# Optimization experiments

Measured on AMD Instinct MI355X. Metric: run time of the kernel, lower is better.

## Reference

```python
import jax, jax.numpy as jnp
import numpy as np

NUM_HEADS = 16
WINDOW = 256
DIM = 1024


def setup_inputs() -> dict:
    key = jax.random.key(0)
    k1, k2, k3, k4, k5 = jax.random.split(key, 5)
    B, L, D = 2, 2048, DIM
    s = 1.0 / np.sqrt(D)
    return {
        "x": jax.random.normal(k1, (B, L, D), dtype=jnp.float32),
        "in_proj_w": jax.random.uniform(k2, (3 * D, D), dtype=jnp.float32, minval=-s, maxval=s),
        "in_proj_b": jax.random.uniform(k3, (3 * D,), dtype=jnp.float32, minval=-s, maxval=s),
        "out_w": jax.random.uniform(k4, (D, D), dtype=jnp.float32, minval=-s, maxval=s),
        "out_b": jax.random.uniform(k5, (D,), dtype=jnp.float32, minval=-s, maxval=s),
    }


def reference(x, in_proj_w, in_proj_b, out_w, out_b):
    B, L, D = x.shape
    H = NUM_HEADS
    hd = D // H

    # combined qkv projection, as in nn.MultiheadAttention
    qkv = x @ in_proj_w.T + in_proj_b          # [B, L, 3D]
    q, k, v = jnp.split(qkv, 3, axis=-1)
    q = q.reshape(B, L, H, hd).transpose(0, 2, 1, 3)  # [B, H, L, hd]
    k = k.reshape(B, L, H, hd).transpose(0, 2, 1, 3)
    v = v.reshape(B, L, H, hd).transpose(0, 2, 1, 3)

    scale = 1.0 / jnp.sqrt(jnp.asarray(hd, dtype=x.dtype))
    scores = jnp.einsum("bhqd,bhkd->bhqk", q * scale, k)  # [B, H, L, L]

    # sliding-window causal mask: allowed iff i-window < j <= i
    i = jnp.arange(L)[:, None]
    j = jnp.arange(L)[None, :]
    allowed = (j <= i) & (j > i - WINDOW)                  # [L, L]
    scores = jnp.where(allowed[None, None], scores, -jnp.inf)

    attn = jax.nn.softmax(scores, axis=-1)
    out = jnp.einsum("bhqk,bhkd->bhqd", attn, v)           # [B, H, L, hd]
    out = out.transpose(0, 2, 1, 3).reshape(B, L, D)
    return out @ out_w.T + out_b
```

## Files before the change

### kernel.cpp

```cpp
#include <hip/hip_runtime.h>


#define SEQ_L 2048
#define WIN   256

typedef __bf16 bf16x8 __attribute__((ext_vector_type(8)));
typedef float  f32x4  __attribute__((ext_vector_type(4)));

__device__ __forceinline__ unsigned short f32_to_bf16(float f) {
  unsigned int u = __float_as_uint(f);
  u += 0x7FFFu + ((u >> 16) & 1u);
  return (unsigned short)(u >> 16);
}

__device__ __forceinline__ void async16(const unsigned short* g, unsigned short* l) {
  __builtin_amdgcn_global_load_lds(
      (const __attribute__((address_space(1))) unsigned int*)g,
      (__attribute__((address_space(3))) unsigned int*)l, 16, 0, 0);
}

__global__ void cast_all(const float* __restrict__ x,  unsigned short* __restrict__ xo,
                         const float* __restrict__ w1, unsigned short* __restrict__ w1o,
                         const float* __restrict__ w2, unsigned short* __restrict__ w2o) {
  int i = blockIdx.x * 256 + threadIdx.x;
  const float* in; unsigned short* out; int k;
  if (i < 1048576)       { in = x;  out = xo;  k = i; }
  else if (i < 1835008)  { in = w1; out = w1o; k = i - 1048576; }
  else                   { in = w2; out = w2o; k = i - 1835008; }
  float4 v = ((const float4*)in)[k];
  ushort4 o;
  o.x = f32_to_bf16(v.x); o.y = f32_to_bf16(v.y);
  o.z = f32_to_bf16(v.z); o.w = f32_to_bf16(v.w);
  ((ushort4*)out)[k] = o;
}

template<int TBM, int TBN, int MI, int NI, int OUTBF>
__global__ __launch_bounds__(256) void gemm_nt(
    const unsigned short* __restrict__ A,
    const unsigned short* __restrict__ Bt,
    const float* __restrict__ bias,
    void* __restrict__ Cout, int M, int N, int K)
{
  __shared__ unsigned short As[TBM * 64];
  __shared__ unsigned short Bs[TBN * 64];

  const int tid  = threadIdx.x;
  const int lane = tid & 63;
  const int wave = tid >> 6;
  const int wr   = (wave >> 1) * (MI * 16);
  const int wc   = (wave & 1) * (NI * 16);
  const int quad = lane >> 4;
  const int l16  = lane & 15;
  const int lrow = lane >> 3;
  const int scol = (lane & 7) ^ lrow;

  const long m0 = (long)blockIdx.y * TBM;
  const long n0 = (long)blockIdx.x * TBN;

  f32x4 acc[MI][NI];
#pragma unroll
  for (int i = 0; i < MI; ++i)
#pragma unroll
    for (int j = 0; j < NI; ++j)
#pragma unroll
      for (int r = 0; r < 4; ++r) acc[i][j][r] = 0.0f;

  for (int k0 = 0; k0 < K; k0 += 64) {
#pragma unroll
    for (int p = 0; p < TBM / 32; ++p) {
      int rb = wave * (TBM / 4) + p * 8;
      async16(A + (m0 + rb + lrow) * (long)K + k0 + scol * 8, &As[rb * 64]);
    }
#pragma unroll
    for (int p = 0; p < TBN / 32; ++p) {
      int rb = wave * (TBN / 4) + p * 8;
      async16(Bt + (n0 + rb + lrow) * (long)K + k0 + scol * 8, &Bs[rb * 64]);
    }
    __syncthreads();
#pragma unroll
    for (int ks = 0; ks < 2; ++ks) {
      bf16x8 af[MI], bfv[NI];
#pragma unroll
      for (int mi = 0; mi < MI; ++mi) {
        int r = wr + mi * 16 + l16;
        af[mi] = *(const bf16x8*)(&As[r * 64 + ((ks * 4 + quad) ^ (r & 7)) * 8]);
      }
#pragma unroll
      for (int ni = 0; ni < NI; ++ni) {
        int r = wc + ni * 16 + l16;
        bfv[ni] = *(const bf16x8*)(&Bs[r * 64 + ((ks * 4 + quad) ^ (r & 7)) * 8]);
      }
#pragma unroll
      for (int mi = 0; mi < MI; ++mi)
#pragma unroll
        for (int ni = 0; ni < NI; ++ni)
          acc[mi][ni] = __builtin_amdgcn_mfma_f32_16x16x32_bf16(af[mi], bfv[ni], acc[mi][ni], 0, 0, 0);
    }
    __syncthreads();
  }

#pragma unroll
  for (int ni = 0; ni < NI; ++ni) {
    long col = n0 + wc + ni * 16 + l16;
    float bv = bias[col];
#pragma unroll
    for (int mi = 0; mi < MI; ++mi) {
      long rowb = m0 + wr + mi * 16 + quad * 4;
#pragma unroll
      for (int r = 0; r < 4; ++r) {
        float v = acc[mi][ni][r] + bv;
        if (OUTBF) ((unsigned short*)Cout)[(rowb + r) * N + col] = f32_to_bf16(v);
        else       ((float*)Cout)[(rowb + r) * N + col] = v;
      }
    }
  }
}

__global__ __launch_bounds__(256) void attn_kernel(
    const unsigned short* __restrict__ qkv,
    unsigned short* __restrict__ aout)
{
  __shared__ unsigned short Ks[64 * 72];
  __shared__ unsigned short Vt[64 * 72];
  __shared__ unsigned short Ps[4 * 16 * 72];

  const int tid  = threadIdx.x;
  const int w    = tid >> 6;
  const int lane = tid & 63;
  const int quad = lane >> 4;
  const int l16  = lane & 15;

  const int blk = blockIdx.x;
  const int qt  = blk & 31;
  const int h   = (blk >> 5) & 15;
  const int b   = blk >> 9;

  const int  i0  = qt * 64;
  const int  i0w = i0 + w * 16;
  const long rowbase = (long)b * SEQ_L;
  const float NEG_INF = -__builtin_inff();

  bf16x8 aq[2];
  {
    const unsigned short* qp = qkv + (rowbase + i0w + l16) * 3072 + h * 64 + quad * 8;
    aq[0] = *(const bf16x8*)(qp);
    aq[1] = *(const bf16x8*)(qp + 32);
  }

  f32x4 o[4];
#pragma unroll
  for (int ni = 0; ni < 4; ++ni)
#pragma unroll
    for (int r = 0; r < 4; ++r) o[ni][r] = 0.0f;
  float m_i[4], l_i[4];
#pragma unroll
  for (int r = 0; r < 4; ++r) { m_i[r] = NEG_INF; l_i[r] = 0.0f; }

  unsigned short* psw = &Ps[w * 16 * 72];

  const int j_begin = (i0 >= WIN) ? i0 - WIN : 0;

  for (int j0 = j_begin; j0 <= i0; j0 += 64) {
    __syncthreads();
#pragma unroll
    for (int p = 0; p < 2; ++p) {
      int c = p * 256 + tid, row = c >> 3, col8 = c & 7;
      const unsigned short* base = qkv + (rowbase + j0 + row) * 3072 + h * 64 + col8 * 8;
      *(uint4*)(&Ks[row * 72 + col8 * 8]) = *(const uint4*)(base + 1024);
      unsigned short tmp[8];
      *(uint4*)tmp = *(const uint4*)(base + 2048);
      int rsw = row ^ (col8 << 3);
#pragma unroll
      for (int e = 0; e < 8; ++e)
        Vt[(col8 * 8 + e) * 72 + rsw] = tmp[e];
    }
    __syncthreads();

    f32x4 s[4];
#pragma unroll
    for (int g = 0; g < 4; ++g) {
      bf16x8 k0 = *(const bf16x8*)(&Ks[(g * 16 + l16) * 72 + quad * 8]);
      bf16x8 k1 = *(const bf16x8*)(&Ks[(g * 16 + l16) * 72 + 32 + quad * 8]);
      f32x4 z;
#pragma unroll
      for (int r = 0; r < 4; ++r) z[r] = 0.0f;
      z = __builtin_amdgcn_mfma_f32_16x16x32_bf16(aq[0], k0, z, 0, 0, 0);
      z = __builtin_amdgcn_mfma_f32_16x16x32_bf16(aq[1], k1, z, 0, 0, 0);
      s[g] = z;
    }
#pragma unroll
    for (int g = 0; g < 4; ++g) {
      int j = j0 + g * 16 + l16;
#pragma unroll
      for (int r = 0; r < 4; ++r) {
        int i = i0w + quad * 4 + r;
        float sv = s[g][r] * 0.125f;
        bool ok = (j <= i) && (j > i - WIN);
        s[g][r] = ok ? sv : NEG_INF;
      }
    }
    float alpha[4];
#pragma unroll
    for (int r = 0; r < 4; ++r) {
      float mx = fmaxf(fmaxf(s[0][r], s[1][r]), fmaxf(s[2][r], s[3][r]));
      mx = fmaxf(mx, __shfl_xor(mx, 1));
      mx = fmaxf(mx, __shfl_xor(mx, 2));
      mx = fmaxf(mx, __shfl_xor(mx, 4));
      mx = fmaxf(mx, __shfl_xor(mx, 8));
      float m_new = fmaxf(m_i[r], mx);
      float a = (m_new == NEG_INF) ? 1.0f : __expf(m_i[r] - m_new);
      float rs = 0.0f;
#pragma unroll
      for (int g = 0; g < 4; ++g) {
        float e = (s[g][r] == NEG_INF) ? 0.0f : __expf(s[g][r] - m_new);
        psw[(quad * 4 + r) * 72 + g * 16 + l16] = f32_to_bf16(e);
        rs += e;
      }
      rs += __shfl_xor(rs, 1);
      rs += __shfl_xor(rs, 2);
      rs += __shfl_xor(rs, 4);
      rs += __shfl_xor(rs, 8);
      l_i[r] = l_i[r] * a + rs;
      m_i[r] = m_new;
      alpha[r] = a;
#pragma unroll
      for (int ni = 0; ni < 4; ++ni) o[ni][r] *= a;
    }
    asm volatile("s_waitcnt lgkmcnt(0)" ::: "memory");
#pragma unroll
    for (int kk = 0; kk < 2; ++kk) {
      bf16x8 ap = *(const bf16x8*)(&psw[l16 * 72 + kk * 32 + quad * 8]);
#pragma unroll
      for (int ni = 0; ni < 4; ++ni) {
        int d  = ni * 16 + l16;
        int rb = (kk * 32 + quad * 8) ^ (((d >> 3) & 7) << 3);
        bf16x8 bv = *(const bf16x8*)(&Vt[d * 72 + rb]);
        o[ni] = __builtin_amdgcn_mfma_f32_16x16x32_bf16(ap, bv, o[ni], 0, 0, 0);
      }
    }
  }

#pragma unroll
  for (int r = 0; r < 4; ++r) {
    float inv_l = 1.0f / l_i[r];
    long row = rowbase + i0w + quad * 4 + r;
#pragma unroll
    for (int ni = 0; ni < 4; ++ni)
      aout[row * 1024 + h * 64 + ni * 16 + l16] = f32_to_bf16(o[ni][r] * inv_l);
  }
}

extern "C" void kernel_launch(void* const* d_in, const int* in_sizes, int n_in,
                              void* d_out, int out_size, void* d_ws, size_t ws_size,
                              hipStream_t stream)
{
  const float* x  = (const float*)d_in[0];
  const float* w1 = (const float*)d_in[1];
  const float* b1 = (const float*)d_in[2];
  const float* w2 = (const float*)d_in[3];
  const float* b2 = (const float*)d_in[4];
  float* out = (float*)d_out;

  char* ws = (char*)d_ws;
  unsigned short* x_bf   = (unsigned short*)(ws);
  unsigned short* w1_bf  = (unsigned short*)(ws + 8388608);
  unsigned short* w2_bf  = (unsigned short*)(ws + 14680064);
  unsigned short* qkv_bf = (unsigned short*)(ws + 16777216);
  unsigned short* at_bf  = (unsigned short*)(ws + 41943040);

  cast_all<<<8192, 256, 0, stream>>>(x, x_bf, w1, w1_bf, w2, w2_bf);

  dim3 g1(3072 / 128, 4096 / 128);
  gemm_nt<128, 128, 4, 4, 1><<<g1, 256, 0, stream>>>(x_bf, w1_bf, b1, qkv_bf, 4096, 3072, 1024);

  attn_kernel<<<1024, 256, 0, stream>>>(qkv_bf, at_bf);

  dim3 g2(1024 / 64, 4096 / 128);
  gemm_nt<128, 64, 4, 2, 0><<<g2, 256, 0, stream>>>(at_bf, w2_bf, b2, out, 4096, 1024, 1024);
}
```

Before: 170.0 us.

## Process two query sub-tiles per attention block, drop online max, retile output GEMM

Each attention block now covers 128 query rows in two 64-row sub-tiles, so every K/V tile loaded into LDS is reused by both sub-tiles and the block count is halved. Fully masked sub-tile/key-tile pairs are skipped. The online softmax max tracking and rescaling are removed and exponentials are taken directly on scaled scores, which relies on the scores staying small enough not to overflow. The output projection GEMM moves to 64x64 tiles, giving more blocks.

Result: faster. 164.1 us (-3.4%).

```diff
diff --git a/kernel.cpp b/kernel.cpp
--- a/kernel.cpp
+++ b/kernel.cpp
@@ -131,36 +131,36 @@
   const int l16  = lane & 15;
 
   const int blk = blockIdx.x;
-  const int qt  = blk & 31;
-  const int h   = (blk >> 5) & 15;
-  const int b   = blk >> 9;
-
-  const int  i0  = qt * 64;
-  const int  i0w = i0 + w * 16;
+  const int qb  = blk & 15;
+  const int h   = (blk >> 4) & 15;
+  const int b   = blk >> 8;
+
+  const int  i0 = qb * 128;
   const long rowbase = (long)b * SEQ_L;
-  const float NEG_INF = -__builtin_inff();
-
-  bf16x8 aq[2];
-  {
-    const unsigned short* qp = qkv + (rowbase + i0w + l16) * 3072 + h * 64 + quad * 8;
-    aq[0] = *(const bf16x8*)(qp);
-    aq[1] = *(const bf16x8*)(qp + 32);
-  }
-
-  f32x4 o[4];
-#pragma unroll
-  for (int ni = 0; ni < 4; ++ni)
-#pragma unroll
-    for (int r = 0; r < 4; ++r) o[ni][r] = 0.0f;
-  float m_i[4], l_i[4];
-#pragma unroll
-  for (int r = 0; r < 4; ++r) { m_i[r] = NEG_INF; l_i[r] = 0.0f; }
+
+  bf16x8 aq[2][2];
+#pragma unroll
+  for (int sub = 0; sub < 2; ++sub) {
+    const unsigned short* qp =
+        qkv + (rowbase + i0 + sub * 64 + w * 16 + l16) * 3072 + h * 64 + quad * 8;
+    aq[sub][0] = *(const bf16x8*)(qp);
+    aq[sub][1] = *(const bf16x8*)(qp + 32);
+  }
+
+  f32x4 o[2][4];
+  float l_i[2][4];
+#pragma unroll
+  for (int sub = 0; sub < 2; ++sub)
+#pragma unroll
+    for (int ni = 0; ni < 4; ++ni)
+#pragma unroll
+      for (int r = 0; r < 4; ++r) { o[sub][ni][r] = 0.0f; l_i[sub][r] = 0.0f; }
 
   unsigned short* psw = &Ps[w * 16 * 72];
 
   const int j_begin = (i0 >= WIN) ? i0 - WIN : 0;
 
-  for (int j0 = j_begin; j0 <= i0; j0 += 64) {
+  for (int j0 = j_begin; j0 < i0 + 128; j0 += 64) {
     __syncthreads();
 #pragma unroll
     for (int p = 0; p < 2; ++p) {
@@ -176,78 +176,76 @@
     }
     __syncthreads();
 
-    f32x4 s[4];
+    bf16x8 kf[4][2];
 #pragma unroll
     for (int g = 0; g < 4; ++g) {
-      bf16x8 k0 = *(const bf16x8*)(&Ks[(g * 16 + l16) * 72 + quad * 8]);
-      bf16x8 k1 = *(const bf16x8*)(&Ks[(g * 16 + l16) * 72 + 32 + quad * 8]);
-      f32x4 z;
-#pragma unroll
-      for (int r = 0; r < 4; ++r) z[r] = 0.0f;
-      z = __builtin_amdgcn_mfma_f32_16x16x32_bf16(aq[0], k0, z, 0, 0, 0);
-      z = __builtin_amdgcn_mfma_f32_16x16x32_bf16(aq[1], k1, z, 0, 0, 0);
-      s[g] = z;
-    }
-#pragma unroll
-    for (int g = 0; g < 4; ++g) {
-      int j = j0 + g * 16 + l16;
-#pragma unroll
-      for (int r = 0; r < 4; ++r) {
-        int i = i0w + quad * 4 + r;
-        float sv = s[g][r] * 0.125f;
-        bool ok = (j <= i) && (j > i - WIN);
-        s[g][r] = ok ? sv : NEG_INF;
-      }
-    }
-    float alpha[4];
+      kf[g][0] = *(const bf16x8*)(&Ks[(g * 16 + l16) * 72 + quad * 8]);
+      kf[g][1] = *(const bf16x8*)(&Ks[(g * 16 + l16) * 72 + 32 + quad * 8]);
+    }
+    bf16x8 vf[2][4];
+#pragma unroll
+    for (int kk = 0; kk < 2; ++kk)
+#pragma unroll
+      for (int ni = 0; ni < 4; ++ni) {
+        int d  = ni * 16 + l16;
+        int rb = (kk * 32 + quad * 8) ^ (((d >> 3) & 7) << 3);
+        vf[kk][ni] = *(const bf16x8*)(&Vt[d * 72 + rb]);
+      }
+
+#pragma unroll
+    for (int sub = 0; sub < 2; ++sub) {
+      const int i0s = i0 + sub * 64 + w * 16;
+      if (j0 > i0s + 15) continue;
+      if (j0 + 63 + WIN <= i0s) continue;
+
+      f32x4 s[4];
+#pragma unroll
+      for (int g = 0; g < 4; ++g) {
+        f32x4 z;
+#pragma unroll
+        for (int r = 0; r < 4; ++r) z[r] = 0.0f;
+        z = __builtin_amdgcn_mfma_f32_16x16x32_bf16(aq[sub][0], kf[g][0], z, 0, 0, 0);
+        z = __builtin_amdgcn_mfma_f32_16x16x32_bf16(aq[sub][1], kf[g][1], z, 0, 0, 0);
+        s[g] = z;
+      }
+#pragma unroll
+      for (int g = 0; g < 4; ++g) {
+        int j = j0 + g * 16 + l16;
+#pragma unroll
+        for (int r = 0; r < 4; ++r) {
+          int i = i0s + quad * 4 + r;
+          bool ok = (j <= i) && (j > i - WIN);
+          float e = ok ? __expf(s[g][r] * 0.125f) : 0.0f;
+          psw[(quad * 4 + r) * 72 + g * 16 + l16] = f32_to_bf16(e);
+          l_i[sub][r] += e;
+        }
+      }
+      asm volatile("s_waitcnt lgkmcnt(0)" ::: "memory");
+#pragma unroll
+      for (int kk = 0; kk < 2; ++kk) {
+        bf16x8 ap = *(const bf16x8*)(&psw[l16 * 72 + kk * 32 + quad * 8]);
+#pragma unroll
+        for (int ni = 0; ni < 4; ++ni)
+          o[sub][ni] = __builtin_amdgcn_mfma_f32_16x16x32_bf16(ap, vf[kk][ni], o[sub][ni], 0, 0, 0);
+      }
+    }
+  }
+
+#pragma unroll
+  for (int sub = 0; sub < 2; ++sub)
 #pragma unroll
     for (int r = 0; r < 4; ++r) {
-      float mx = fmaxf(fmaxf(s[0][r], s[1][r]), fmaxf(s[2][r], s[3][r]));
-      mx = fmaxf(mx, __shfl_xor(mx, 1));
-      mx = fmaxf(mx, __shfl_xor(mx, 2));
-      mx = fmaxf(mx, __shfl_xor(mx, 4));
-      mx = fmaxf(mx, __shfl_xor(mx, 8));
-      float m_new = fmaxf(m_i[r], mx);
-      float a = (m_new == NEG_INF) ? 1.0f : __expf(m_i[r] - m_new);
-      float rs = 0.0f;
-#pragma unroll
-      for (int g = 0; g < 4; ++g) {
-        float e = (s[g][r] == NEG_INF) ? 0.0f : __expf(s[g][r] - m_new);
-        psw[(quad * 4 + r) * 72 + g * 16 + l16] = f32_to_bf16(e);
-        rs += e;
-      }
+      float rs = l_i[sub][r];
       rs += __shfl_xor(rs, 1);
       rs += __shfl_xor(rs, 2);
       rs += __shfl_xor(rs, 4);
       rs += __shfl_xor(rs, 8);
-      l_i[r] = l_i[r] * a + rs;
-      m_i[r] = m_new;
-      alpha[r] = a;
-#pragma unroll
-      for (int ni = 0; ni < 4; ++ni) o[ni][r] *= a;
-    }
-    asm volatile("s_waitcnt lgkmcnt(0)" ::: "memory");
-#pragma unroll
-    for (int kk = 0; kk < 2; ++kk) {
-      bf16x8 ap = *(const bf16x8*)(&psw[l16 * 72 + kk * 32 + quad * 8]);
-#pragma unroll
-      for (int ni = 0; ni < 4; ++ni) {
-        int d  = ni * 16 + l16;
-        int rb = (kk * 32 + quad * 8) ^ (((d >> 3) & 7) << 3);
-        bf16x8 bv = *(const bf16x8*)(&Vt[d * 72 + rb]);
-        o[ni] = __builtin_amdgcn_mfma_f32_16x16x32_bf16(ap, bv, o[ni], 0, 0, 0);
-      }
-    }
-  }
-
-#pragma unroll
-  for (int r = 0; r < 4; ++r) {
-    float inv_l = 1.0f / l_i[r];
-    long row = rowbase + i0w + quad * 4 + r;
-#pragma unroll
-    for (int ni = 0; ni < 4; ++ni)
-      aout[row * 1024 + h * 64 + ni * 16 + l16] = f32_to_bf16(o[ni][r] * inv_l);
-  }
+      float inv_l = 1.0f / rs;
+      long row = rowbase + i0 + sub * 64 + w * 16 + quad * 4 + r;
+#pragma unroll
+      for (int ni = 0; ni < 4; ++ni)
+        aout[row * 1024 + h * 64 + ni * 16 + l16] = f32_to_bf16(o[sub][ni][r] * inv_l);
+    }
 }
 
 extern "C" void kernel_launch(void* const* d_in, const int* in_sizes, int n_in,
@@ -273,8 +271,8 @@
   dim3 g1(3072 / 128, 4096 / 128);
   gemm_nt<128, 128, 4, 4, 1><<<g1, 256, 0, stream>>>(x_bf, w1_bf, b1, qkv_bf, 4096, 3072, 1024);
 
-  attn_kernel<<<1024, 256, 0, stream>>>(qkv_bf, at_bf);
-
-  dim3 g2(1024 / 64, 4096 / 128);
-  gemm_nt<128, 64, 4, 2, 0><<<g2, 256, 0, stream>>>(at_bf, w2_bf, b2, out, 4096, 1024, 1024);
-}
+  attn_kernel<<<512, 256, 0, stream>>>(qkv_bf, at_bf);
+
+  dim3 g2(1024 / 64, 4096 / 64);
+  gemm_nt<64, 64, 2, 2, 0><<<g2, 256, 0, stream>>>(at_bf, w2_bf, b2, out, 4096, 1024, 1024);
+}
```
